# Performance work log

Measured on AMD Instinct MI355X. Metric: run time of the kernel, lower is better.

## Reference

```python
import jax, jax.numpy as jnp
import numpy as np
from jax.scipy.linalg import solve_triangular

OMEGA0 = 30.0  # standard SIREN first-layer frequency


def setup_inputs() -> dict:
    key = jax.random.key(0)
    ks = jax.random.split(key, 12)
    B, NC, NT, XD, H, R = 64, 1024, 1024, 1, 512, 512
    x_context = jax.random.normal(ks[0], (B, NC, XD), jnp.float32)
    y_context = jax.random.normal(ks[1], (B, NC, 1), jnp.float32)
    x_target = jax.random.normal(ks[2], (B, NT, XD), jnp.float32)
    # SIREN MLP params (hidden_dims=[512,512,512], repr_dim=512)
    def lin(k, fi, fo, first=False):
        bound = 1.0 / fi if first else np.sqrt(6.0 / fi) / OMEGA0
        kW, kb = jax.random.split(k)
        W = jax.random.uniform(kW, (fi, fo), jnp.float32, -bound, bound)
        b = jax.random.uniform(kb, (fo,), jnp.float32, -bound, bound)
        return W, b
    W0, b0 = lin(ks[3], XD, H, first=True)
    W1, b1 = lin(ks[4], H, H)
    W2, b2 = lin(ks[5], H, H)
    Wr, br = lin(ks[6], H, R)
    log_noise_var = jnp.asarray(np.log(0.01), jnp.float32)
    return {"x_context": x_context, "y_context": y_context, "x_target": x_target,
            "W0": W0, "b0": b0, "W1": W1, "b1": b1, "W2": W2, "b2": b2,
            "Wr": Wr, "br": br, "log_noise_var": log_noise_var}


def _mlp(x, W0, b0, W1, b1, W2, b2, Wr, br):
    # SIREN: sine activations, omega_0 on first layer, linear head
    h = jnp.sin(OMEGA0 * (x @ W0 + b0))
    h = jnp.sin(h @ W1 + b1)
    h = jnp.sin(h @ W2 + b2)
    return h @ Wr + br


def reference(x_context, y_context, x_target, W0, b0, W1, b1, W2, b2, Wr, br, log_noise_var):
    mean = jnp.mean(y_context, axis=1, keepdims=True)          # [B,1,1]
    std = jnp.std(y_context, axis=1, keepdims=True, ddof=1)    # torch.std is unbiased
    yc = (y_context - mean) / std                              # [B,N,1]

    cr = _mlp(x_context, W0, b0, W1, b1, W2, b2, Wr, br)       # [B,N,R]
    tr = _mlp(x_target, W0, b0, W1, b1, W2, b2, Wr, br)        # [B,M,R]
    ones_c = jnp.ones(cr.shape[:-1] + (1,), cr.dtype)
    ones_t = jnp.ones(tr.shape[:-1] + (1,), tr.dtype)
    cr = jnp.concatenate([cr, ones_c], axis=-1)                # [B,N,R+1]
    tr = jnp.concatenate([tr, ones_t], axis=-1)                # [B,M,R+1]

    Rp1 = cr.shape[-1]
    cov = jnp.einsum('bnr,bns->brs', cr, cr)                   # [B,R+1,R+1]
    cov = cov + jnp.exp(log_noise_var) * jnp.eye(Rp1, dtype=cov.dtype)
    xty = jnp.einsum('bnr,bnd->brd', cr, yc)                   # [B,R+1,1]

    chol = jnp.linalg.cholesky(cov)                            # batched potrf
    z = solve_triangular(chol, xty, lower=True)
    w = solve_triangular(jnp.swapaxes(chol, -1, -2), z, lower=False)  # [B,R+1,1]

    y_pred = tr @ w                                            # [B,M,1]
    return y_pred * std + mean
```

## Files before the change

kernel.cpp:

```cpp
#include <hip/hip_runtime.h>
#include <hip/hip_fp16.h>
#include <math.h>

#define NB    64
#define NPTS  1024
#define HD    512
#define CPAD  576
#define COVE  ((size_t)NB*CPAD*CPAD)

typedef __attribute__((ext_vector_type(4))) float v4f;
typedef __attribute__((ext_vector_type(8))) short v8s;
typedef __attribute__((ext_vector_type(8))) _Float16 v8h;

__device__ __forceinline__ float sin_poly(float z){
  float t = z*z;
  float p = fmaf(t, -1.9841270e-4f, 8.3333333e-3f);
  p = fmaf(t, p, -0.16666667f);
  p = fmaf(t, p, 1.0f);
  return z*p;
}

__device__ __forceinline__ ushort2 split_f16(float a){
  _Float16 h = (_Float16)a;
  float hf = (float)h;
  _Float16 l = (_Float16)(a - hf);
  unsigned short uh, ul;
  __builtin_memcpy(&uh, &h, 2);
  __builtin_memcpy(&ul, &l, 2);
  ushort2 r; r.x = uh; r.y = ul;
  return r;
}

__device__ __forceinline__ unsigned short f16b(float a){
  _Float16 h = (_Float16)a;
  unsigned short uh; __builtin_memcpy(&uh, &h, 2);
  return uh;
}

__device__ __forceinline__ float f16r(float a){
  return (float)(_Float16)a;
}

__global__ __launch_bounds__(256)
void prep_k(const float* __restrict__ W1, const float* __restrict__ W2,
            const float* __restrict__ Wr, unsigned short* __restrict__ wf)
{
  int idx = blockIdx.x*256 + threadIdx.x;
  int mat = idx >> 18;
  int rem = idx & 0x3ffff;
  int k = rem >> 9, n = rem & 511;
  const float* W = (mat==0) ? W1 : ((mat==1) ? W2 : Wr);
  wf[(size_t)mat*262144 + (size_t)n*512 + k] = f16b(W[(size_t)k*512 + n]);
}

template<int AMODE>
__device__ __forceinline__ void load_a(const unsigned short* __restrict__ Ap,
                                       size_t ga0, size_t ga1, int K0,
                                       const float* __restrict__ w0,
                                       const float* __restrict__ b0, int sq,
                                       float xv0, float xv1,
                                       v8s& pa0, v8s& pa1)
{
  if (AMODE == 0){
    pa0 = *(const v8s*)(Ap + ga0 + K0); pa1 = *(const v8s*)(Ap + ga1 + K0);
  } else {
    const float* wp = w0 + K0 + sq*8;
    const float* bp = b0 + K0 + sq*8;
    float4 wva = *(const float4*)wp, wvb = *(const float4*)(wp+4);
    float4 bva = *(const float4*)bp, bvb = *(const float4*)(bp+4);
    float w8[8] = {wva.x,wva.y,wva.z,wva.w,wvb.x,wvb.y,wvb.z,wvb.w};
    float b8[8] = {bva.x,bva.y,bva.z,bva.w,bvb.x,bvb.y,bvb.z,bvb.w};
    #pragma unroll
    for (int i=0;i<8;++i){
      pa0[i] = (short)f16b(__sinf(30.f*fmaf(xv0, w8[i], b8[i])));
      pa1[i] = (short)f16b(__sinf(30.f*fmaf(xv1, w8[i], b8[i])));
    }
  }
}

template<int EPI, int TRANS, int AMODE>
__global__ __launch_bounds__(256)
void gemm_ld(const unsigned short* __restrict__ Ap,
             const float* __restrict__ xsrc, const float* __restrict__ w0,
             const float* __restrict__ b0,
             const unsigned short* __restrict__ Bw,
             const float* __restrict__ bias,
             unsigned short* __restrict__ Chi, unsigned short* __restrict__ Clo,
             const float* __restrict__ vvp, float* __restrict__ ydot, int rowBase)
{
  __shared__ unsigned short Ah[128*40], Bh[128*40];
  const int tid  = threadIdx.x;
  const int lane = tid & 63, wave = tid >> 6;
  const int wm = wave & 1, wn = wave >> 1;
  const int m0 = blockIdx.x*128, n0 = blockIdx.y*128;
  const int q = lane >> 4, ln16 = lane & 15;
  const int sr = tid >> 2, sq = tid & 3;

  const size_t ga0 = (size_t)(m0 + sr)*512 + sq*8;
  const size_t ga1 = ga0 + (size_t)64*512;
  const size_t gb0 = (size_t)(n0 + sr)*512 + sq*8;
  const size_t gb1 = gb0 + (size_t)64*512;

  float xv0 = 0.f, xv1 = 0.f;
  if (AMODE == 1){ xv0 = xsrc[m0 + sr]; xv1 = xsrc[m0 + sr + 64]; }

  v8s pa0, pa1, pb0, pb1;
#define BLOAD(K0) do { \
    pb0 = *(const v8s*)(Bw + gb0 + (K0)); pb1 = *(const v8s*)(Bw + gb1 + (K0)); \
  } while(0)
#define STASH() do { \
    *(v8s*)(Ah + sr*40 + sq*8) = pa0; *(v8s*)(Ah + (sr+64)*40 + sq*8) = pa1; \
    *(v8s*)(Bh + sr*40 + sq*8) = pb0; *(v8s*)(Bh + (sr+64)*40 + sq*8) = pb1; \
  } while(0)

  v4f acc[4][4];
  #pragma unroll
  for (int a=0;a<4;++a)
    #pragma unroll
    for (int b=0;b<4;++b) acc[a][b] = (v4f)(0.0f);

  load_a<AMODE>(Ap, ga0, ga1, 0, w0, b0, sq, xv0, xv1, pa0, pa1);
  BLOAD(0);
  for (int ks=0; ks<16; ++ks){
    STASH();
    __syncthreads();
    if (ks < 15){
      const int k1 = (ks+1)*32;
      load_a<AMODE>(Ap, ga0, ga1, k1, w0, b0, sq, xv0, xv1, pa0, pa1);
      BLOAD(k1);
    }
    v8h bhf[4];
    #pragma unroll
    for (int nt=0; nt<4; ++nt){
      const int nrow = wn*64 + nt*16 + ln16;
      bhf[nt] = *(const v8h*)(Bh + nrow*40 + q*8);
    }
    #pragma unroll
    for (int mt=0; mt<4; ++mt){
      const int mrow = wm*64 + mt*16 + ln16;
      v8h ah = *(const v8h*)(Ah + mrow*40 + q*8);
      #pragma unroll
      for (int nt=0; nt<4; ++nt)
        acc[mt][nt] = __builtin_amdgcn_mfma_f32_16x16x32_f16(ah, bhf[nt], acc[mt][nt], 0,0,0);
    }
    __syncthreads();
  }
#undef BLOAD
#undef STASH

  if (TRANS == 0){
    #pragma unroll
    for (int nt=0;nt<4;++nt){
      const int col = n0 + wn*64 + nt*16 + ln16;
      const float bl_ = bias[col];
      #pragma unroll
      for (int mt=0;mt<4;++mt){
        const int row0 = m0 + wm*64 + mt*16 + q*4;
        #pragma unroll
        for (int r=0;r<4;++r){
          float v = acc[mt][nt][r] + bl_;
          if (EPI == 1) v = sin_poly(v);
          Chi[(size_t)(row0+r)*512 + col] = f16b(v);
        }
      }
    }
  } else if (TRANS == 1){
    const int lb = m0 >> 10;
    #pragma unroll
    for (int nt=0;nt<4;++nt){
      const int col = n0 + wn*64 + nt*16 + ln16;
      const float bl_ = bias[col];
      #pragma unroll
      for (int mt=0;mt<4;++mt){
        const int row0 = m0 + wm*64 + mt*16 + q*4;
        const int nb = row0 & 1023;
        ushort4 h,l; ushort2 s;
        s=split_f16(acc[mt][nt][0]+bl_); h.x=s.x; l.x=s.y;
        s=split_f16(acc[mt][nt][1]+bl_); h.y=s.x; l.y=s.y;
        s=split_f16(acc[mt][nt][2]+bl_); h.z=s.x; l.z=s.y;
        s=split_f16(acc[mt][nt][3]+bl_); h.w=s.x; l.w=s.y;
        size_t o = ((size_t)lb*512 + col)*1024 + nb;
        *(ushort4*)(Chi + o) = h;
        *(ushort4*)(Clo + o) = l;
      }
    }
  } else {
    const int b = (rowBase + m0) >> 10;
    const float* vb = vvp + (size_t)b*512;
    float vcol[4];
    float bl_[4];
    #pragma unroll
    for (int nt=0;nt<4;++nt){
      const int col = n0 + wn*64 + nt*16 + ln16;
      vcol[nt] = vb[col];
      bl_[nt] = bias[col];
    }
    #pragma unroll
    for (int mt=0;mt<4;++mt){
      #pragma unroll
      for (int r=0;r<4;++r){
        float part = 0.f;
        #pragma unroll
        for (int nt=0;nt<4;++nt)
          part = fmaf(sin_poly(acc[mt][nt][r] + bl_[nt]), vcol[nt], part);
        #pragma unroll
        for (int off=1; off<16; off<<=1) part += __shfl_xor(part, off, 64);
        if (ln16 == 0){
          const int row = m0 + wm*64 + mt*16 + q*4 + r;
          atomicAdd(&ydot[rowBase + row], part);
        }
      }
    }
  }
}

__device__ __forceinline__ void ld_ext_row(const unsigned short* __restrict__ h,
                                           const unsigned short* __restrict__ l,
                                           const float* __restrict__ ycn,
                                           int f, int nofs, v8s& oh, v8s& ol)
{
  if (f < 512){
    oh = *(const v8s*)(h + (size_t)f*1024 + nofs);
    ol = *(const v8s*)(l + (size_t)f*1024 + nofs);
  } else if (f == 512){
    #pragma unroll
    for (int j=0;j<8;++j){ oh[j] = (short)0x3C00; ol[j] = 0; }
  } else if (f == 513){
    #pragma unroll
    for (int j=0;j<8;++j){
      ushort2 s = split_f16(ycn[nofs+j]);
      oh[j] = (short)s.x; ol[j] = (short)s.y;
    }
  } else {
    #pragma unroll
    for (int j=0;j<8;++j){ oh[j] = 0; ol[j] = 0; }
  }
}

__global__ __launch_bounds__(256)
void cov_ld(const unsigned short* __restrict__ CThi, const unsigned short* __restrict__ CTlo,
            const float* __restrict__ ycb,
            const float* __restrict__ lnv, float* __restrict__ cov, int bStart)
{
  int t = blockIdx.x;
  int ti = 0;
  while ((ti+1)*(ti+2)/2 <= t) ++ti;
  int tj = t - ti*(ti+1)/2;
  const int i0 = ti*128, j0 = tj*128;
  const int lb = blockIdx.y;
  const int b  = bStart + lb;
  const unsigned short* srch = CThi + (size_t)lb*512*1024;
  const unsigned short* srcl = CTlo + (size_t)lb*512*1024;
  const float* ycn = ycb + (size_t)b*NPTS;
  float* covb = cov + (size_t)b*CPAD*CPAD;
  const float noise = expf(lnv[0]);
  const bool diag = (i0 == j0);

  __shared__ unsigned short Ah[128*40], Al[128*40], Bh2[128*40], Bl2[128*40];
  const int tid = threadIdx.x;
  const int lane = tid & 63, wave = tid >> 6;
  const int wm = wave & 1, wn = wave >> 1;
  const int q = lane >> 4, ln16 = lane & 15;
  const int sr = tid >> 2, sq = tid & 3;

  const int fA0 = i0 + sr, fA1 = i0 + sr + 64;
  const int fB0 = j0 + sr, fB1 = j0 + sr + 64;

  v8s pah0, pah1, pal0, pal1, pbh0, pbh1, pbl0, pbl1;

  v4f acc[4][4];
  #pragma unroll
  for (int a=0;a<4;++a)
    #pragma unroll
    for (int c=0;c<4;++c) acc[a][c] = (v4f)(0.0f);

  ld_ext_row(srch, srcl, ycn, fA0, sq*8, pah0, pal0);
  ld_ext_row(srch, srcl, ycn, fA1, sq*8, pah1, pal1);
  if (!diag){
    ld_ext_row(srch, srcl, ycn, fB0, sq*8, pbh0, pbl0);
    ld_ext_row(srch, srcl, ycn, fB1, sq*8, pbh1, pbl1);
  }
  for (int ks=0; ks<32; ++ks){
    *(v8s*)(Ah + sr*40 + sq*8) = pah0; *(v8s*)(Ah + (sr+64)*40 + sq*8) = pah1;
    *(v8s*)(Al + sr*40 + sq*8) = pal0; *(v8s*)(Al + (sr+64)*40 + sq*8) = pal1;
    if (!diag){
      *(v8s*)(Bh2 + sr*40 + sq*8) = pbh0; *(v8s*)(Bh2 + (sr+64)*40 + sq*8) = pbh1;
      *(v8s*)(Bl2 + sr*40 + sq*8) = pbl0; *(v8s*)(Bl2 + (sr+64)*40 + sq*8) = pbl1;
    }
    __syncthreads();
    if (ks < 31){
      const int n1 = (ks+1)*32 + sq*8;
      ld_ext_row(srch, srcl, ycn, fA0, n1, pah0, pal0);
      ld_ext_row(srch, srcl, ycn, fA1, n1, pah1, pal1);
      if (!diag){
        ld_ext_row(srch, srcl, ycn, fB0, n1, pbh0, pbl0);
        ld_ext_row(srch, srcl, ycn, fB1, n1, pbh1, pbl1);
      }
    }
    const unsigned short* BhP = diag ? Ah : Bh2;
    const unsigned short* BlP = diag ? Al : Bl2;
    v8h bhf[4], blf[4];
    #pragma unroll
    for (int nt=0; nt<4; ++nt){
      const int nrow = wn*64 + nt*16 + ln16;
      bhf[nt] = *(const v8h*)(BhP + nrow*40 + q*8);
      blf[nt] = *(const v8h*)(BlP + nrow*40 + q*8);
    }
    #pragma unroll
    for (int mt=0; mt<4; ++mt){
      const int mrow = wm*64 + mt*16 + ln16;
      v8h ah = *(const v8h*)(Ah + mrow*40 + q*8);
      v8h al = *(const v8h*)(Al + mrow*40 + q*8);
      #pragma unroll
      for (int nt=0; nt<4; ++nt){
        acc[mt][nt] = __builtin_amdgcn_mfma_f32_16x16x32_f16(ah, bhf[nt], acc[mt][nt], 0,0,0);
        acc[mt][nt] = __builtin_amdgcn_mfma_f32_16x16x32_f16(ah, blf[nt], acc[mt][nt], 0,0,0);
        acc[mt][nt] = __builtin_amdgcn_mfma_f32_16x16x32_f16(al, bhf[nt], acc[mt][nt], 0,0,0);
      }
    }
    __syncthreads();
  }
  #pragma unroll
  for (int nt=0;nt<4;++nt){
    const int gj = j0 + wn*64 + nt*16 + ln16;
    #pragma unroll
    for (int mt=0;mt<4;++mt){
      const int gi0 = i0 + wm*64 + mt*16 + q*4;
      #pragma unroll
      for (int r=0;r<4;++r){
        const int gi = gi0 + r;
        if (gj <= gi && gi < CPAD && gj < CPAD){
          float v = acc[mt][nt][r];
          if (gi == gj) v += (gi < 513) ? noise : 1.0f;
          covb[(size_t)gi*CPAD + gj] = v;
        }
      }
    }
  }
}

__global__ __launch_bounds__(256)
void chol_trsm_k(float* __restrict__ cov, float* __restrict__ dchol, int k)
{
  (void)dchol;
  float* Ab = cov + (size_t)blockIdx.x * CPAD * CPAD;
  const int o = k*64;
  const int row0 = o + 64 + blockIdx.y*128;
  const int nrows = min(128, CPAD - row0);
  __shared__ float Ds[64][65];
  __shared__ float As[128][65];
  __shared__ float invd[64];
  const int tid = threadIdx.x;

  for (int idx=tid; idx<1024; idx+=256){
    int r = idx >> 4, c = (idx & 15)*4;
    float4 v = *(const float4*)(Ab + (size_t)(o+r)*CPAD + o + c);
    Ds[r][c]   = (c   <= r) ? v.x : 0.f;
    Ds[r][c+1] = (c+1 <= r) ? v.y : 0.f;
    Ds[r][c+2] = (c+2 <= r) ? v.z : 0.f;
    Ds[r][c+3] = (c+3 <= r) ? v.w : 0.f;
  }
  for (int idx=tid; idx<nrows*16; idx+=256){
    int r = idx >> 4, c = (idx & 15)*4;
    float4 v = *(const float4*)(Ab + (size_t)(row0+r)*CPAD + o + c);
    As[r][c]=v.x; As[r][c+1]=v.y; As[r][c+2]=v.z; As[r][c+3]=v.w;
  }
  __syncthreads();

  for (int j=0; j<64; ++j){
    const float rp = 1.0f / Ds[j][j];
    const int i = j + 1 + (tid & 63);
    if (i < 64){
      const float t = Ds[i][j] * rp;
      for (int c = j+1+(tid>>6); c <= i; c += 4)
        Ds[i][c] = fmaf(-t, Ds[c][j], Ds[i][c]);
    }
    __syncthreads();
  }
  if (tid < 64) invd[tid] = 1.0f / sqrtf(Ds[tid][tid]);
  __syncthreads();
  for (int idx=tid; idx<4096; idx+=256){
    int r = idx >> 6, c = idx & 63;
    if (c <= r) Ds[r][c] *= invd[c];
  }
  __syncthreads();

  if (tid < nrows){
    float x[64];
    #pragma unroll
    for (int c=0; c<64; ++c){
      float s0 = As[tid][c], s1 = 0.f, s2 = 0.f, s3 = 0.f;
      #pragma unroll
      for (int j=0; j+4<=c; j+=4){
        s0 = fmaf(-x[j],   Ds[c][j],   s0);
        s1 = fmaf(-x[j+1], Ds[c][j+1], s1);
        s2 = fmaf(-x[j+2], Ds[c][j+2], s2);
        s3 = fmaf(-x[j+3], Ds[c][j+3], s3);
      }
      #pragma unroll
      for (int j = c & ~3; j < c; ++j)
        s0 = fmaf(-x[j], Ds[c][j], s0);
      x[c] = ((s0+s1)+(s2+s3)) * invd[c];
    }
    #pragma unroll
    for (int c=0; c<64; ++c) As[tid][c] = x[c];
  } else if (blockIdx.y == 0 && tid >= 128 && tid < 192){
    const int r = tid - 128;
    float y[64];
    #pragma unroll
    for (int c = 63; c >= 0; --c){
      float s0 = (c == r) ? 1.0f : 0.0f, s1 = 0.f, s2 = 0.f, s3 = 0.f;
      #pragma unroll
      for (int j = c+1; j+4 <= 64; j += 4){
        s0 = fmaf(-Ds[j][c],   y[j],   s0);
        s1 = fmaf(-Ds[j+1][c], y[j+1], s1);
        s2 = fmaf(-Ds[j+2][c], y[j+2], s2);
        s3 = fmaf(-Ds[j+3][c], y[j+3], s3);
      }
      #pragma unroll
      for (int j = c+1 + ((63-c) & ~3); j < 64; ++j)
        s0 = fmaf(-Ds[j][c], y[j], s0);
      y[c] = ((s0+s1)+(s2+s3)) * invd[c];
    }
    float* dst = Ab + (size_t)(o + r)*CPAD + 512;
    #pragma unroll
    for (int c = 0; c < 64; c += 4)
      *(float4*)(dst + c) = make_float4(y[c], y[c+1], y[c+2], y[c+3]);
  }
  __syncthreads();
  for (int idx=tid; idx<nrows*16; idx+=256){
    int r = idx >> 4, c = (idx & 15)*4;
    float4 v = make_float4(As[r][c], As[r][c+1], As[r][c+2], As[r][c+3]);
    *(float4*)(Ab + (size_t)(row0+r)*CPAD + o + c) = v;
  }
}

__global__ __launch_bounds__(256)
void chol_trail_k(float* __restrict__ cov, int k)
{
  float* Ab = cov + (size_t)blockIdx.y * CPAD * CPAD;
  int t = blockIdx.x;
  int bi = 0;
  while ((bi+1)*(bi+2)/2 <= t) ++bi;
  int bj = t - bi*(bi+1)/2;
  const int o = k*64;
  const int s0 = o + 64;
  const int I = s0 + bi*64, J = s0 + bj*64;

  __shared__ float Pi[64*64];
  __shared__ float Pj[64*64];
  const int tid = threadIdx.x;
  for (int idx = tid; idx < 1024; idx += 256){
    int r = idx >> 4, cq = idx & 15;
    float4 v = *(const float4*)(Ab + (size_t)(I+r)*CPAD + o + cq*4);
    Pi[(cq*4+0)*64 + r] = v.x; Pi[(cq*4+1)*64 + r] = v.y;
    Pi[(cq*4+2)*64 + r] = v.z; Pi[(cq*4+3)*64 + r] = v.w;
    float4 u = *(const float4*)(Ab + (size_t)(J+r)*CPAD + o + cq*4);
    Pj[(cq*4+0)*64 + r] = u.x; Pj[(cq*4+1)*64 + r] = u.y;
    Pj[(cq*4+2)*64 + r] = u.z; Pj[(cq*4+3)*64 + r] = u.w;
  }
  __syncthreads();
  const int tx = tid & 15, ty = tid >> 4;
  float acc[4][4];
  #pragma unroll
  for (int r=0;r<4;++r)
    #pragma unroll
    for (int c=0;c<4;++c) acc[r][c]=0.f;
  for (int kk=0; kk<64; ++kk){
    float4 a4 = *(const float4*)(Pi + kk*64 + tx*4);
    float4 b4 = *(const float4*)(Pj + kk*64 + ty*4);
    float av[4]={a4.x,a4.y,a4.z,a4.w}, bv[4]={b4.x,b4.y,b4.z,b4.w};
    #pragma unroll
    for (int r=0;r<4;++r)
      #pragma unroll
      for (int c=0;c<4;++c) acc[r][c] = fmaf(av[r], bv[c], acc[r][c]);
  }
  #pragma unroll
  for (int r=0;r<4;++r){
    int gi = I + tx*4 + r;
    #pragma unroll
    for (int c=0;c<4;++c){
      int gj = J + ty*4 + c;
      if (gj <= gi){
        size_t id = (size_t)gi*CPAD + gj;
        Ab[id] -= acc[r][c];
      }
    }
  }
}

__global__ __launch_bounds__(256)
void chol_last_k(float* __restrict__ cov, float* __restrict__ dchol)
{
  float* Ab = cov + (size_t)blockIdx.x * CPAD * CPAD;
  __shared__ float P[64][65];
  __shared__ float Ds[64][65];
  __shared__ float invl[64];
  const int tid = threadIdx.x;

  for (int idx=tid; idx<1024; idx+=256){
    int r = idx >> 4, c = (idx & 15)*4;
    float4 v = *(const float4*)(Ab + (size_t)(512+r)*CPAD + 448 + c);
    P[r][c]=v.x; P[r][c+1]=v.y; P[r][c+2]=v.z; P[r][c+3]=v.w;
    float4 u = *(const float4*)(Ab + (size_t)(512+r)*CPAD + 512 + c);
    Ds[r][c]   = (c   <= r) ? u.x : 0.f;
    Ds[r][c+1] = (c+1 <= r) ? u.y : 0.f;
    Ds[r][c+2] = (c+2 <= r) ? u.z : 0.f;
    Ds[r][c+3] = (c+3 <= r) ? u.w : 0.f;
  }
  __syncthreads();
  {
    const int tx = tid & 15, ty = tid >> 4;
    float acc[4][4];
    #pragma unroll
    for (int r=0;r<4;++r)
      #pragma unroll
      for (int c=0;c<4;++c) acc[r][c]=0.f;
    for (int kk=0; kk<64; ++kk){
      float av[4], bv[4];
      #pragma unroll
      for (int r=0;r<4;++r) av[r] = P[tx*4+r][kk];
      #pragma unroll
      for (int c=0;c<4;++c) bv[c] = P[ty*4+c][kk];
      #pragma unroll
      for (int r=0;r<4;++r)
        #pragma unroll
        for (int c=0;c<4;++c) acc[r][c] = fmaf(av[r], bv[c], acc[r][c]);
    }
    __syncthreads();
    #pragma unroll
    for (int r=0;r<4;++r){
      int gi = tx*4 + r;
      #pragma unroll
      for (int c=0;c<4;++c){
        int gj = ty*4 + c;
        if (gj <= gi) Ds[gi][gj] -= acc[r][c];
      }
    }
  }
  __syncthreads();

  for (int j=0; j<64; ++j){
    const float rp = 1.0f / Ds[j][j];
    const int i = j + 1 + (tid & 63);
    if (i < 64){
      const float t = Ds[i][j] * rp;
      for (int c = j+1+(tid>>6); c <= i; c += 4)
        Ds[i][c] = fmaf(-t, Ds[c][j], Ds[i][c]);
    }
    __syncthreads();
  }
  if (tid < 64) invl[tid] = 1.0f / sqrtf(Ds[tid][tid]);
  __syncthreads();
  for (int idx=tid; idx<4096; idx+=256){
    int r = idx >> 6, c = idx & 63;
    if (c <= r) Ds[r][c] *= invl[c];
  }
  __syncthreads();

  float* dst = dchol + ((size_t)blockIdx.x*9 + 8)*4096;
  for (int idx=tid; idx<4096; idx+=256)
    dst[idx] = Ds[idx>>6][idx&63];
  if (tid < 64){
    const int r = tid;
    float y[64];
    #pragma unroll
    for (int c = 63; c >= 0; --c){
      float s0 = (c == r) ? 1.0f : 0.0f, s1 = 0.f, s2 = 0.f, s3 = 0.f;
      #pragma unroll
      for (int j = c+1; j+4 <= 64; j += 4){
        s0 = fmaf(-Ds[j][c],   y[j],   s0);
        s1 = fmaf(-Ds[j+1][c], y[j+1], s1);
        s2 = fmaf(-Ds[j+2][c], y[j+2], s2);
        s3 = fmaf(-Ds[j+3][c], y[j+3], s3);
      }
      #pragma unroll
      for (int j = c+1 + ((63-c) & ~3); j < 64; ++j)
        s0 = fmaf(-Ds[j][c], y[j], s0);
      y[c] = ((s0+s1)+(s2+s3)) * invl[c];
    }
    float* dst2 = Ab + (size_t)(512 + r)*CPAD + 512;
    #pragma unroll
    for (int c = 0; c < 64; c += 4)
      *(float4*)(dst2 + c) = make_float4(y[c], y[c+1], y[c+2], y[c+3]);
  }
}

__global__ __launch_bounds__(1024)
void back_solve_k(const float* __restrict__ cov, const float* __restrict__ dchol,
                  float* __restrict__ wv)
{
  const int b = blockIdx.x;
  const float* L = cov + (size_t)b*CPAD*CPAD;
  const float* dc = dchol + (size_t)b*9*4096;
  __shared__ float inv2[64*64];
  __shared__ float rhs[CPAD];
  __shared__ float xv[64];
  __shared__ float red[4*512];
  const int tid = threadIdx.x;
  const int pr = tid >> 4, pc = (tid & 15)*4;
  const float* zrow = L + (size_t)513*CPAD;

  for (int i=tid; i<CPAD; i+=1024)
    rhs[i] = (i < 512) ? zrow[i] : ((i == 512) ? dc[8*4096 + 64] : 0.f);
  {
    float4 v = *(const float4*)(L + (size_t)(512 + pr)*CPAD + 512 + pc);
    *(float4*)(inv2 + pr*64 + pc) = v;
  }
  __syncthreads();

  for (int k=8; k>=1; --k){
    const int o = k*64;
    const int G = o >> 2;
    const int act = G << 2;
    float4 v16[16];
    int rg = 0, cg = 0;
    if (tid < act){
      rg = tid / G; cg = tid % G;
      const float* lp = L + (size_t)(o + rg*16)*CPAD + cg*4;
      #pragma unroll
      for (int rr=0; rr<16; ++rr)
        v16[rr] = *(const float4*)(lp + (size_t)rr*CPAD);
    }
    float4 pf = *(const float4*)(L + (size_t)((k-1)*64 + pr)*CPAD + 512 + pc);
    if (tid < 64){
      float acc = 0.f;
      #pragma unroll
      for (int j=0;j<64;++j) acc = fmaf(inv2[j*64 + tid], rhs[o+j], acc);
      xv[tid] = acc;
      rhs[o+tid] = acc;
    }
    __syncthreads();
    if (tid < act){
      float4 s = {0.f,0.f,0.f,0.f};
      #pragma unroll
      for (int rr=0; rr<16; ++rr){
        float xr = xv[rg*16 + rr];
        s.x = fmaf(v16[rr].x, xr, s.x);
        s.y = fmaf(v16[rr].y, xr, s.y);
        s.z = fmaf(v16[rr].z, xr, s.z);
        s.w = fmaf(v16[rr].w, xr, s.w);
      }
      *(float4*)(red + rg*512 + cg*4) = s;
    }
    __syncthreads();
    if (tid < o)
      rhs[tid] -= (red[tid] + red[512+tid]) + (red[1024+tid] + red[1536+tid]);
    *(float4*)(inv2 + pr*64 + pc) = pf;
    __syncthreads();
  }
  if (tid < 64){
    float acc = 0.f;
    #pragma unroll
    for (int j=0;j<64;++j) acc = fmaf(inv2[j*64 + tid], rhs[j], acc);
    rhs[tid] = acc;
  }
  __syncthreads();
  for (int i=tid; i<CPAD; i+=1024) wv[(size_t)b*CPAD + i] = rhs[i];
}

__global__ __launch_bounds__(512)
void fold_k(const float* __restrict__ Wr, const float* __restrict__ br,
            const float* __restrict__ wv, float* __restrict__ vv, float* __restrict__ cvec)
{
  int b = blockIdx.x, j = threadIdx.x;
  const float* wb = wv + (size_t)b*CPAD;
  __shared__ float ws_[512];
  __shared__ float red[512];
  ws_[j] = wb[j];
  __syncthreads();
  float acc = 0.f;
  const float* row = Wr + (size_t)j*512;
  for (int r=0; r<512; r+=4){
    float4 w4 = *(const float4*)(row + r);
    acc = fmaf(f16r(w4.x), ws_[r],   acc);
    acc = fmaf(f16r(w4.y), ws_[r+1], acc);
    acc = fmaf(f16r(w4.z), ws_[r+2], acc);
    acc = fmaf(f16r(w4.w), ws_[r+3], acc);
  }
  vv[(size_t)b*512 + j] = acc;
  red[j] = br[j]*ws_[j];
  __syncthreads();
  for (int s=256; s>0; s>>=1){ if (j<s) red[j]+=red[j+s]; __syncthreads(); }
  if (j == 0) cvec[b] = red[0] + wb[512];
}

__global__ __launch_bounds__(256)
void stats_k(const float* __restrict__ y, float* __restrict__ meanv,
             float* __restrict__ stdv, float* __restrict__ ycb)
{
  int b = blockIdx.x, tid = threadIdx.x;
  const float* yb = y + (size_t)b*NPTS;
  float4 v = *(const float4*)(yb + tid*4);
  float s  = v.x+v.y+v.z+v.w;
  float ss = v.x*v.x+v.y*v.y+v.z*v.z+v.w*v.w;
  #pragma unroll
  for (int off=32; off; off>>=1){ s += __shfl_down(s, off); ss += __shfl_down(ss, off); }
  __shared__ float rs[4], rss[4], bc[2];
  int wid = tid>>6, lane = tid&63;
  if (lane == 0){ rs[wid]=s; rss[wid]=ss; }
  __syncthreads();
  if (tid == 0){
    float S  = rs[0]+rs[1]+rs[2]+rs[3];
    float SS = rss[0]+rss[1]+rss[2]+rss[3];
    float mean = S * (1.0f/NPTS);
    float var  = (SS - S*S*(1.0f/NPTS)) * (1.0f/(NPTS-1));
    float sd = sqrtf(var);
    meanv[b]=mean; stdv[b]=sd; bc[0]=mean; bc[1]=1.0f/sd;
  }
  __syncthreads();
  float mean=bc[0], inv=bc[1];
  float4 o;
  o.x=(v.x-mean)*inv; o.y=(v.y-mean)*inv; o.z=(v.z-mean)*inv; o.w=(v.w-mean)*inv;
  *(float4*)(ycb + (size_t)b*NPTS + tid*4) = o;
}

__global__ __launch_bounds__(256)
void fin_k(const float* __restrict__ ydot, const float* __restrict__ cvec,
           const float* __restrict__ meanv, const float* __restrict__ stdv,
           float* __restrict__ out)
{
  int i = blockIdx.x*256 + threadIdx.x;
  int b = i >> 10;
  out[i] = fmaf(ydot[i] + cvec[b], stdv[b], meanv[b]);
}

extern "C" void kernel_launch(void* const* d_in, const int* in_sizes, int n_in,
                              void* d_out, int out_size, void* d_ws, size_t ws_size,
                              hipStream_t stream)
{
  (void)in_sizes; (void)n_in; (void)out_size;
  const float* x_ctx = (const float*)d_in[0];
  const float* y_ctx = (const float*)d_in[1];
  const float* x_tgt = (const float*)d_in[2];
  const float* W0 = (const float*)d_in[3];
  const float* b0 = (const float*)d_in[4];
  const float* W1 = (const float*)d_in[5];
  const float* b1 = (const float*)d_in[6];
  const float* W2 = (const float*)d_in[7];
  const float* b2 = (const float*)d_in[8];
  const float* Wr = (const float*)d_in[9];
  const float* br = (const float*)d_in[10];
  const float* lnv = (const float*)d_in[11];
  float* out = (float*)d_out;
  float* ws = (float*)d_ws;

  int CH = 65536;
  for (;;){
    size_t fl = COVE + 65536 + 192 + (size_t)64*512 + (size_t)64*CPAD + 65536
              + (size_t)64*9*4096 + 64;
    size_t sh = (size_t)3*262144 + (size_t)2*CH*512 + (size_t)2*(CH/1024)*512*1024;
    size_t need = fl*4 + sh*2;
    if (ws_size >= need || CH <= 1024) break;
    CH >>= 1;
  }
  const int nch = 65536 / CH;
  const int bpc = CH / NPTS;

  float* cov   = ws;
  float* ycb   = cov + COVE;
  float* meanv = ycb + 65536;
  float* stdv  = meanv + 64;
  float* cvec  = stdv + 64;
  float* vvb   = cvec + 64;
  float* wvb   = vvb + (size_t)64*512;
  float* ydot  = wvb + (size_t)64*CPAD;
  float* dchol = ydot + 65536;
  unsigned short* wf   = (unsigned short*)(dchol + (size_t)64*9*4096);
  unsigned short* P0   = wf + (size_t)3*262144;
  unsigned short* P1   = P0 + (size_t)CH*512;
  unsigned short* CThi = P1 + (size_t)CH*512;
  unsigned short* CTlo = CThi + (size_t)bpc*512*1024;

  prep_k<<<3072, 256, 0, stream>>>(W1, W2, Wr, wf);
  stats_k<<<NB, 256, 0, stream>>>(y_ctx, meanv, stdv, ycb);

  for (int c=0; c<nch; ++c){
    const float* xc = x_ctx + (size_t)c*CH;
    dim3 g(CH/128, 4);
    gemm_ld<1,0,1><<<g, 256, 0, stream>>>(0, xc, W0, b0, wf, b1, P1, 0, 0, 0, 0);
    gemm_ld<1,0,0><<<g, 256, 0, stream>>>(P1, 0, 0, 0, wf+262144, b2, P0, 0, 0, 0, 0);
    gemm_ld<0,1,0><<<g, 256, 0, stream>>>(P0, 0, 0, 0, wf+524288, br, CThi, CTlo, 0, 0, 0);
    cov_ld<<<dim3(15, bpc), 256, 0, stream>>>(CThi, CTlo, ycb, lnv, cov, c*bpc);
  }

  for (int k=0; k<8; ++k){
    const int cnt = CPAD - k*64 - 64;
    chol_trsm_k<<<dim3(NB, (cnt + 127)/128), 256, 0, stream>>>(cov, dchol, k);
    if (k < 7){
      const int tcnt = cnt >> 6;
      chol_trail_k<<<dim3(tcnt*(tcnt+1)/2, NB), 256, 0, stream>>>(cov, k);
    }
  }
  chol_last_k<<<NB, 256, 0, stream>>>(cov, dchol);
  back_solve_k<<<NB, 1024, 0, stream>>>(cov, dchol, wvb);
  fold_k<<<NB, 512, 0, stream>>>(Wr, br, wvb, vvb, cvec);

  hipMemsetAsync(ydot, 0, 65536*sizeof(float), stream);
  for (int c=0; c<nch; ++c){
    const float* xt = x_tgt + (size_t)c*CH;
    dim3 g(CH/128, 4);
    gemm_ld<1,0,1><<<g, 256, 0, stream>>>(0, xt, W0, b0, wf, b1, P1, 0, 0, 0, 0);
    gemm_ld<1,2,0><<<g, 256, 0, stream>>>(P1, 0, 0, 0, wf+262144, b2, 0, 0, vvb, ydot, c*CH);
  }
  fin_k<<<256, 256, 0, stream>>>(ydot, cvec, meanv, stdv, out);
}
```

Baseline: 1.320 ms.

## Use direct global-to-LDS loads in GEMM and covariance kernels; tile weight transpose

Replaces the register-staged global loads and LDS stores in the MLP GEMM and covariance kernels with global_load_lds DMA into unpadded LDS tiles. The software prefetch into registers is removed, and the extra bias row block in cov_ld keeps a register path. The weight transpose kernel now goes through a shared-memory tile so both its reads and writes are coalesced. In exchange, the unpadded 32-element row stride may cause LDS bank conflicts, and global latency is no longer overlapped with MFMA work, since loads are issued and then waited on in the same iteration.

Measured after the change: 1.312 ms. Within noise of the previous version (-0.6%).

```diff
diff --git a/kernel.cpp b/kernel.cpp
--- a/kernel.cpp
+++ b/kernel.cpp
@@ -41,40 +41,48 @@
   return (float)(_Float16)a;
 }
 
+__device__ __forceinline__ void g2l16(const unsigned short* g, unsigned short* l){
+  __builtin_amdgcn_global_load_lds(
+      (const __attribute__((address_space(1))) unsigned int*)(g),
+      (__attribute__((address_space(3))) unsigned int*)(l), 16, 0, 0);
+}
+
 __global__ __launch_bounds__(256)
 void prep_k(const float* __restrict__ W1, const float* __restrict__ W2,
             const float* __restrict__ Wr, unsigned short* __restrict__ wf)
 {
-  int idx = blockIdx.x*256 + threadIdx.x;
-  int mat = idx >> 18;
-  int rem = idx & 0x3ffff;
-  int k = rem >> 9, n = rem & 511;
+  __shared__ unsigned short tile[64][65];
+  const int mat = blockIdx.x >> 6;
+  const int t = blockIdx.x & 63;
+  const int k0 = (t >> 3)*64, n0 = (t & 7)*64;
   const float* W = (mat==0) ? W1 : ((mat==1) ? W2 : Wr);
-  wf[(size_t)mat*262144 + (size_t)n*512 + k] = f16b(W[(size_t)k*512 + n]);
-}
-
-template<int AMODE>
-__device__ __forceinline__ void load_a(const unsigned short* __restrict__ Ap,
-                                       size_t ga0, size_t ga1, int K0,
-                                       const float* __restrict__ w0,
-                                       const float* __restrict__ b0, int sq,
-                                       float xv0, float xv1,
-                                       v8s& pa0, v8s& pa1)
-{
-  if (AMODE == 0){
-    pa0 = *(const v8s*)(Ap + ga0 + K0); pa1 = *(const v8s*)(Ap + ga1 + K0);
-  } else {
-    const float* wp = w0 + K0 + sq*8;
-    const float* bp = b0 + K0 + sq*8;
-    float4 wva = *(const float4*)wp, wvb = *(const float4*)(wp+4);
-    float4 bva = *(const float4*)bp, bvb = *(const float4*)(bp+4);
-    float w8[8] = {wva.x,wva.y,wva.z,wva.w,wvb.x,wvb.y,wvb.z,wvb.w};
-    float b8[8] = {bva.x,bva.y,bva.z,bva.w,bvb.x,bvb.y,bvb.z,bvb.w};
-    #pragma unroll
-    for (int i=0;i<8;++i){
-      pa0[i] = (short)f16b(__sinf(30.f*fmaf(xv0, w8[i], b8[i])));
-      pa1[i] = (short)f16b(__sinf(30.f*fmaf(xv1, w8[i], b8[i])));
-    }
+  const int tid = threadIdx.x;
+  for (int idx=tid; idx<4096; idx+=256){
+    int r = idx >> 6, c = idx & 63;
+    tile[r][c] = f16b(W[(size_t)(k0+r)*512 + n0 + c]);
+  }
+  __syncthreads();
+  unsigned short* dst = wf + (size_t)mat*262144;
+  for (int idx=tid; idx<4096; idx+=256){
+    int r = idx >> 6, c = idx & 63;
+    dst[(size_t)(n0+r)*512 + k0 + c] = tile[c][r];
+  }
+}
+
+__device__ __forceinline__ void h0c(const float* __restrict__ w0,
+                                    const float* __restrict__ b0, int K0, int sq,
+                                    float xv0, float xv1, v8s& pa0, v8s& pa1)
+{
+  const float* wp = w0 + K0 + sq*8;
+  const float* bp = b0 + K0 + sq*8;
+  float4 wva = *(const float4*)wp, wvb = *(const float4*)(wp+4);
+  float4 bva = *(const float4*)bp, bvb = *(const float4*)(bp+4);
+  float w8[8] = {wva.x,wva.y,wva.z,wva.w,wvb.x,wvb.y,wvb.z,wvb.w};
+  float b8[8] = {bva.x,bva.y,bva.z,bva.w,bvb.x,bvb.y,bvb.z,bvb.w};
+  #pragma unroll
+  for (int i=0;i<8;++i){
+    pa0[i] = (short)f16b(__sinf(30.f*fmaf(xv0, w8[i], b8[i])));
+    pa1[i] = (short)f16b(__sinf(30.f*fmaf(xv1, w8[i], b8[i])));
   }
 }
 
@@ -88,7 +96,7 @@
              unsigned short* __restrict__ Chi, unsigned short* __restrict__ Clo,
              const float* __restrict__ vvp, float* __restrict__ ydot, int rowBase)
 {
-  __shared__ unsigned short Ah[128*40], Bh[128*40];
+  __shared__ unsigned short Ah[128*32], Bh[128*32];
   const int tid  = threadIdx.x;
   const int lane = tid & 63, wave = tid >> 6;
   const int wm = wave & 1, wn = wave >> 1;
@@ -96,22 +104,14 @@
   const int q = lane >> 4, ln16 = lane & 15;
   const int sr = tid >> 2, sq = tid & 3;
 
-  const size_t ga0 = (size_t)(m0 + sr)*512 + sq*8;
-  const size_t ga1 = ga0 + (size_t)64*512;
-  const size_t gb0 = (size_t)(n0 + sr)*512 + sq*8;
-  const size_t gb1 = gb0 + (size_t)64*512;
+  const int strow = wave*32 + (lane>>2);
+  const unsigned short* gA = Ap + (size_t)(m0 + strow)*512 + (lane&3)*8;
+  const unsigned short* gB = Bw + (size_t)(n0 + strow)*512 + (lane&3)*8;
+  unsigned short* lA0 = Ah + wave*1024;
+  unsigned short* lB0 = Bh + wave*1024;
 
   float xv0 = 0.f, xv1 = 0.f;
   if (AMODE == 1){ xv0 = xsrc[m0 + sr]; xv1 = xsrc[m0 + sr + 64]; }
-
-  v8s pa0, pa1, pb0, pb1;
-#define BLOAD(K0) do { \
-    pb0 = *(const v8s*)(Bw + gb0 + (K0)); pb1 = *(const v8s*)(Bw + gb1 + (K0)); \
-  } while(0)
-#define STASH() do { \
-    *(v8s*)(Ah + sr*40 + sq*8) = pa0; *(v8s*)(Ah + (sr+64)*40 + sq*8) = pa1; \
-    *(v8s*)(Bh + sr*40 + sq*8) = pb0; *(v8s*)(Bh + (sr+64)*40 + sq*8) = pb1; \
-  } while(0)
 
   v4f acc[4][4];
   #pragma unroll
@@ -119,34 +119,38 @@
     #pragma unroll
     for (int b=0;b<4;++b) acc[a][b] = (v4f)(0.0f);
 
-  load_a<AMODE>(Ap, ga0, ga1, 0, w0, b0, sq, xv0, xv1, pa0, pa1);
-  BLOAD(0);
+  v8s pa0, pa1;
+  if (AMODE == 1) h0c(w0, b0, 0, sq, xv0, xv1, pa0, pa1);
+
   for (int ks=0; ks<16; ++ks){
-    STASH();
+    const int k0 = ks*32;
+    if (ks) __syncthreads();
+    if (AMODE == 0){
+      g2l16(gA + k0, lA0); g2l16(gA + k0 + 16*512, lA0 + 512);
+    } else {
+      *(v8s*)(Ah + sr*32 + sq*8) = pa0;
+      *(v8s*)(Ah + (sr+64)*32 + sq*8) = pa1;
+    }
+    g2l16(gB + k0, lB0); g2l16(gB + k0 + 16*512, lB0 + 512);
     __syncthreads();
-    if (ks < 15){
-      const int k1 = (ks+1)*32;
-      load_a<AMODE>(Ap, ga0, ga1, k1, w0, b0, sq, xv0, xv1, pa0, pa1);
-      BLOAD(k1);
-    }
+    if (AMODE == 1 && ks < 15)
+      h0c(w0, b0, k0+32, sq, xv0, xv1, pa0, pa1);
+
     v8h bhf[4];
     #pragma unroll
     for (int nt=0; nt<4; ++nt){
       const int nrow = wn*64 + nt*16 + ln16;
-      bhf[nt] = *(const v8h*)(Bh + nrow*40 + q*8);
+      bhf[nt] = *(const v8h*)(Bh + nrow*32 + q*8);
     }
     #pragma unroll
     for (int mt=0; mt<4; ++mt){
       const int mrow = wm*64 + mt*16 + ln16;
-      v8h ah = *(const v8h*)(Ah + mrow*40 + q*8);
+      v8h ah = *(const v8h*)(Ah + mrow*32 + q*8);
       #pragma unroll
       for (int nt=0; nt<4; ++nt)
         acc[mt][nt] = __builtin_amdgcn_mfma_f32_16x16x32_f16(ah, bhf[nt], acc[mt][nt], 0,0,0);
     }
-    __syncthreads();
-  }
-#undef BLOAD
-#undef STASH
+  }
 
   if (TRANS == 0){
     #pragma unroll
@@ -255,18 +259,22 @@
   float* covb = cov + (size_t)b*CPAD*CPAD;
   const float noise = expf(lnv[0]);
   const bool diag = (i0 == j0);
-
-  __shared__ unsigned short Ah[128*40], Al[128*40], Bh2[128*40], Bl2[128*40];
+  const bool aReg = (i0 == 512);
+
+  __shared__ unsigned short Ah[128*32], Al[128*32], Bh2[128*32], Bl2[128*32];
   const int tid = threadIdx.x;
   const int lane = tid & 63, wave = tid >> 6;
   const int wm = wave & 1, wn = wave >> 1;
   const int q = lane >> 4, ln16 = lane & 15;
   const int sr = tid >> 2, sq = tid & 3;
 
-  const int fA0 = i0 + sr, fA1 = i0 + sr + 64;
-  const int fB0 = j0 + sr, fB1 = j0 + sr + 64;
-
-  v8s pah0, pah1, pal0, pal1, pbh0, pbh1, pbl0, pbl1;
+  const int strow = wave*32 + (lane>>2);
+  const size_t gaOff = (size_t)(i0 + strow)*1024 + (lane&3)*8;
+  const size_t gbOff = (size_t)(j0 + strow)*1024 + (lane&3)*8;
+  unsigned short* lA0 = Ah  + wave*1024;
+  unsigned short* lL0 = Al  + wave*1024;
+  unsigned short* lB0 = Bh2 + wave*1024;
+  unsigned short* lM0 = Bl2 + wave*1024;
 
   v4f acc[4][4];
   #pragma unroll
@@ -274,43 +282,39 @@
     #pragma unroll
     for (int c=0;c<4;++c) acc[a][c] = (v4f)(0.0f);
 
-  ld_ext_row(srch, srcl, ycn, fA0, sq*8, pah0, pal0);
-  ld_ext_row(srch, srcl, ycn, fA1, sq*8, pah1, pal1);
-  if (!diag){
-    ld_ext_row(srch, srcl, ycn, fB0, sq*8, pbh0, pbl0);
-    ld_ext_row(srch, srcl, ycn, fB1, sq*8, pbh1, pbl1);
-  }
   for (int ks=0; ks<32; ++ks){
-    *(v8s*)(Ah + sr*40 + sq*8) = pah0; *(v8s*)(Ah + (sr+64)*40 + sq*8) = pah1;
-    *(v8s*)(Al + sr*40 + sq*8) = pal0; *(v8s*)(Al + (sr+64)*40 + sq*8) = pal1;
+    const int k0 = ks*32;
+    if (ks) __syncthreads();
+    if (!aReg){
+      g2l16(srch + gaOff + k0, lA0); g2l16(srch + gaOff + k0 + (size_t)16*1024, lA0 + 512);
+      g2l16(srcl + gaOff + k0, lL0); g2l16(srcl + gaOff + k0 + (size_t)16*1024, lL0 + 512);
+    } else {
+      v8s th, tl;
+      ld_ext_row(srch, srcl, ycn, i0 + sr, k0 + sq*8, th, tl);
+      *(v8s*)(Ah + sr*32 + sq*8) = th; *(v8s*)(Al + sr*32 + sq*8) = tl;
+      ld_ext_row(srch, srcl, ycn, i0 + sr + 64, k0 + sq*8, th, tl);
+      *(v8s*)(Ah + (sr+64)*32 + sq*8) = th; *(v8s*)(Al + (sr+64)*32 + sq*8) = tl;
+    }
     if (!diag){
-      *(v8s*)(Bh2 + sr*40 + sq*8) = pbh0; *(v8s*)(Bh2 + (sr+64)*40 + sq*8) = pbh1;
-      *(v8s*)(Bl2 + sr*40 + sq*8) = pbl0; *(v8s*)(Bl2 + (sr+64)*40 + sq*8) = pbl1;
+      g2l16(srch + gbOff + k0, lB0); g2l16(srch + gbOff + k0 + (size_t)16*1024, lB0 + 512);
+      g2l16(srcl + gbOff + k0, lM0); g2l16(srcl + gbOff + k0 + (size_t)16*1024, lM0 + 512);
     }
     __syncthreads();
-    if (ks < 31){
-      const int n1 = (ks+1)*32 + sq*8;
-      ld_ext_row(srch, srcl, ycn, fA0, n1, pah0, pal0);
-      ld_ext_row(srch, srcl, ycn, fA1, n1, pah1, pal1);
-      if (!diag){
-        ld_ext_row(srch, srcl, ycn, fB0, n1, pbh0, pbl0);
-        ld_ext_row(srch, srcl, ycn, fB1, n1, pbh1, pbl1);
-      }
-    }
+
     const unsigned short* BhP = diag ? Ah : Bh2;
     const unsigned short* BlP = diag ? Al : Bl2;
     v8h bhf[4], blf[4];
     #pragma unroll
     for (int nt=0; nt<4; ++nt){
       const int nrow = wn*64 + nt*16 + ln16;
-      bhf[nt] = *(const v8h*)(BhP + nrow*40 + q*8);
-      blf[nt] = *(const v8h*)(BlP + nrow*40 + q*8);
+      bhf[nt] = *(const v8h*)(BhP + nrow*32 + q*8);
+      blf[nt] = *(const v8h*)(BlP + nrow*32 + q*8);
     }
     #pragma unroll
     for (int mt=0; mt<4; ++mt){
       const int mrow = wm*64 + mt*16 + ln16;
-      v8h ah = *(const v8h*)(Ah + mrow*40 + q*8);
-      v8h al = *(const v8h*)(Al + mrow*40 + q*8);
+      v8h ah = *(const v8h*)(Ah + mrow*32 + q*8);
+      v8h al = *(const v8h*)(Al + mrow*32 + q*8);
       #pragma unroll
       for (int nt=0; nt<4; ++nt){
         acc[mt][nt] = __builtin_amdgcn_mfma_f32_16x16x32_f16(ah, bhf[nt], acc[mt][nt], 0,0,0);
@@ -318,7 +322,6 @@
         acc[mt][nt] = __builtin_amdgcn_mfma_f32_16x16x32_f16(al, bhf[nt], acc[mt][nt], 0,0,0);
       }
     }
-    __syncthreads();
   }
   #pragma unroll
   for (int nt=0;nt<4;++nt){
@@ -772,7 +775,7 @@
   unsigned short* CThi = P1 + (size_t)CH*512;
   unsigned short* CTlo = CThi + (size_t)bpc*512*1024;
 
-  prep_k<<<3072, 256, 0, stream>>>(W1, W2, Wr, wf);
+  prep_k<<<192, 256, 0, stream>>>(W1, W2, Wr, wf);
   stats_k<<<NB, 256, 0, stream>>>(y_ctx, meanv, stdv, ycb);
 
   for (int c=0; c<nch; ++c){
```
